# Optimization experiments

Measured on AMD Instinct MI355X. Metric: run time of the kernel, lower is better.

## Reference

```python
import jax, jax.numpy as jnp
import numpy as np
from jax import lax

B, L, C = 8, 2048, 512
H = 8
D = C // H  # head_dim = 64
FF = 4 * C


def layer_norm(x, g, b, eps=1e-5):
    mu = jnp.mean(x, axis=-1, keepdims=True)
    var = jnp.mean((x - mu) ** 2, axis=-1, keepdims=True)
    return (x - mu) * lax.rsqrt(var + eps) * g + b


def conv1d(x, w, b, groups=1):
    # x: [N, Cin, L], w: [Cout, Cin//groups, K], 'same' padding for K=3
    y = lax.conv_general_dilated(
        x, w, window_strides=(1,), padding=[(1, 1)],
        dimension_numbers=('NCH', 'OIH', 'NCH'), feature_group_count=groups)
    return y + b[None, :, None]


def setup_inputs() -> dict:
    key = jax.random.key(0)
    ks = jax.random.split(key, 12)
    s = 0.02
    inp = {
        'x': jax.random.normal(ks[0], (B, L, C), dtype=jnp.float32),
        # norm1
        'g1': jnp.ones((C,), jnp.float32), 'b1': jnp.zeros((C,), jnp.float32),
        # attention projections (stored as [in, out] for x @ W)
        'qk_w': jax.random.normal(ks[1], (C, 2 * C), jnp.float32) * s,
        'qk_b': jnp.zeros((2 * C,), jnp.float32),
        'v_w': jax.random.normal(ks[2], (C, C), jnp.float32) * s,
        'v_b': jnp.zeros((C,), jnp.float32),
        # depthwise LePE conv: [D, 1, 3], groups=D
        'lepe_w': jax.random.normal(ks[3], (D, 1, 3), jnp.float32) * s,
        'lepe_b': jnp.zeros((D,), jnp.float32),
        # norm2
        'g2': jnp.ones((C,), jnp.float32), 'b2': jnp.zeros((C,), jnp.float32),
        # GatedConv1D: inner LayerNorm + Conv1d(C, 2C, 3, pad=1); proj_out=Identity (expansion=1)
        'spn_g': jnp.ones((C,), jnp.float32), 'spn_b': jnp.zeros((C,), jnp.float32),
        'sp_cw': jax.random.normal(ks[4], (2 * C, C, 3), jnp.float32) * s,
        'sp_cb': jnp.zeros((2 * C,), jnp.float32),
        # norm3
        'g3': jnp.ones((C,), jnp.float32), 'b3': jnp.zeros((C,), jnp.float32),
        # FFN
        'w1': jax.random.normal(ks[5], (C, FF), jnp.float32) * s,
        'bb1': jnp.zeros((FF,), jnp.float32),
        'w2': jax.random.normal(ks[6], (FF, C), jnp.float32) * s,
        'bb2': jnp.zeros((C,), jnp.float32),
    }
    return inp


def _attn(x, qk_w, qk_b, v_w, v_b, lepe_w, lepe_b):
    # x: [B, L, C]
    qk = (x @ qk_w + qk_b).reshape(B, L, 2, H, D).transpose(2, 0, 3, 1, 4)
    q, k = qk[0], qk[1]                      # [B, H, L, D]
    v = (x @ v_w + v_b).reshape(B, L, H, D).transpose(0, 2, 1, 3)  # [B, H, L, D]
    q = jax.nn.elu(q) + 1.0
    k = jax.nn.elu(k) + 1.0

    def lepe(t):
        # Faithful to torch: raw row-major reshape [B,H,L,D] -> [B*H, D, L]
        # (NOT a transpose), depthwise conv along last axis, reshape back.
        c = conv1d(t.reshape(B * H, D, L), lepe_w, lepe_b, groups=D)
        return t + c.reshape(B, H, D, L).transpose(0, 1, 3, 2)

    q = lepe(q)
    k = lepe(k)
    k_mean = jnp.mean(k, axis=2, keepdims=True)                    # [B, H, 1, D]
    z = 1.0 / (jnp.einsum('bhld,bhmd->bhlm', q, k_mean) + 1e-6)    # [B, H, L, 1]
    kv = jnp.einsum('bhld,bhle->bhde', k, v) / L                   # [B, H, D, D]
    out = jnp.einsum('bhld,bhde->bhle', q, kv) * z                 # [B, H, L, D]
    return out.transpose(0, 2, 1, 3).reshape(B, L, C)


def reference(x, g1, b1, qk_w, qk_b, v_w, v_b, lepe_w, lepe_b,
              g2, b2, spn_g, spn_b, sp_cw, sp_cb, g3, b3, w1, bb1, w2, bb2):
    # Dropout is identity (eval mode).
    # Block 1: linear attention with LePE
    x = x + _attn(layer_norm(x, g1, b1), qk_w, qk_b, v_w, v_b, lepe_w, lepe_b)

    # Block 2: gated conv state path. state_path(input) = input + gated(conv(LN(input)))
    sp_in = layer_norm(x, g2, b2)
    h = layer_norm(sp_in, spn_g, spn_b)
    c = conv1d(h.transpose(0, 2, 1), sp_cw, sp_cb).transpose(0, 2, 1)  # [B, L, 2C]
    vv, gg = jnp.split(c, 2, axis=-1)
    x = x + (sp_in + vv * jax.nn.sigmoid(gg))

    # Block 3: FFN with exact GELU (torch default)
    h = layer_norm(x, g3, b3)
    x = x + (jax.nn.gelu(h @ w1 + bb1, approximate=False) @ w2 + bb2)
    return x
```

## Files before the change

### kernel.cpp

```cpp
#include <hip/hip_runtime.h>
#include <hip/hip_bf16.h>
#include <math.h>

#define Bb 8
#define Ll 2048
#define Ccn 512
#define Hh 8
#define Dd 64
#define NR (Bb * Ll)

typedef __hip_bfloat16 bf16;
typedef __attribute__((ext_vector_type(8))) __bf16 bf16x8;
typedef __attribute__((ext_vector_type(4))) float f32x4;

#define GLDS(g, l) __builtin_amdgcn_global_load_lds(                          \
    (const __attribute__((address_space(1))) void*)(g),                       \
    (__attribute__((address_space(3))) void*)(l), 16, 0, 0)

__device__ __forceinline__ void unpack2(unsigned u, float& a, float& b) {
  union { float f; unsigned x; } lo, hi;
  lo.x = u << 16; hi.x = u & 0xffff0000u;
  a = lo.f; b = hi.f;
}

__device__ __forceinline__ float ldin(const void* p, int i, int isbf) {
  return isbf ? (float)((const bf16*)p)[i] : ((const float*)p)[i];
}

__device__ __forceinline__ void ldin8(const void* p, size_t base, int isbf, float* v) {
  if (isbf) {
    int4 q = *(const int4*)((const bf16*)p + base);
    unpack2((unsigned)q.x, v[0], v[1]); unpack2((unsigned)q.y, v[2], v[3]);
    unpack2((unsigned)q.z, v[4], v[5]); unpack2((unsigned)q.w, v[6], v[7]);
  } else {
    float4 a = *(const float4*)((const float*)p + base);
    float4 b = *(const float4*)((const float*)p + base + 4);
    v[0]=a.x; v[1]=a.y; v[2]=a.z; v[3]=a.w;
    v[4]=b.x; v[5]=b.y; v[6]=b.z; v[7]=b.w;
  }
}

__device__ __forceinline__ void st8(bf16* dst, const float* v) {
  bf16x8 o;
#pragma unroll
  for (int t = 0; t < 8; ++t) o[t] = (__bf16)v[t];
  *(bf16x8*)dst = o;
}

__global__ void detect_kernel(const unsigned* __restrict__ g1, int* __restrict__ flag) {
  *flag = ((g1[0] & 0xFFFFu) == 0x3F80u) ? 1 : 0;
}

__global__ void ln1_kernel(const void* __restrict__ x, const void* __restrict__ g,
                           const void* __restrict__ b, const int* __restrict__ dflag,
                           bf16* __restrict__ outb, float* __restrict__ xf)
{
  int isbf = *dflag;
  int row  = blockIdx.x * 4 + (threadIdx.x >> 6);
  int lane = threadIdx.x & 63;
  size_t obase = (size_t)row * Ccn + lane * 8;
  float vals[8];
  ldin8(x, obase, isbf, vals);
  float4 c0 = {vals[0], vals[1], vals[2], vals[3]};
  float4 c1 = {vals[4], vals[5], vals[6], vals[7]};
  *(float4*)(xf + obase)     = c0;
  *(float4*)(xf + obase + 4) = c1;
  float s = 0.f, q = 0.f;
#pragma unroll
  for (int a = 0; a < 8; ++a) { s += vals[a]; q += vals[a] * vals[a]; }
#pragma unroll
  for (int off = 1; off < 64; off <<= 1) {
    s += __shfl_xor(s, off);
    q += __shfl_xor(q, off);
  }
  float mu  = s * (1.f / Ccn);
  float var = q * (1.f / Ccn) - mu * mu;
  float rs  = rsqrtf(var + 1e-5f);
  float gv[8], bv[8], o[8];
  ldin8(g, lane * 8, isbf, gv);
  ldin8(b, lane * 8, isbf, bv);
#pragma unroll
  for (int a = 0; a < 8; ++a) o[a] = (vals[a] - mu) * rs * gv[a] + bv[a];
  st8(&outb[obase], o);
}

__global__ void ln_kernel(const float* __restrict__ xin, const void* __restrict__ g,
                          const void* __restrict__ b, const int* __restrict__ dflag,
                          bf16* __restrict__ outb)
{
  int isbf = *dflag;
  int row  = blockIdx.x * 4 + (threadIdx.x >> 6);
  int lane = threadIdx.x & 63;
  const float* xr = xin + (size_t)row * Ccn;
  float4 v0 = *(const float4*)(xr + lane * 8);
  float4 v1 = *(const float4*)(xr + lane * 8 + 4);
  float vals[8] = {v0.x, v0.y, v0.z, v0.w, v1.x, v1.y, v1.z, v1.w};
  float s = 0.f, q = 0.f;
#pragma unroll
  for (int a = 0; a < 8; ++a) { s += vals[a]; q += vals[a] * vals[a]; }
#pragma unroll
  for (int off = 1; off < 64; off <<= 1) {
    s += __shfl_xor(s, off);
    q += __shfl_xor(q, off);
  }
  float mu  = s * (1.f / Ccn);
  float var = q * (1.f / Ccn) - mu * mu;
  float rs  = rsqrtf(var + 1e-5f);
  size_t obase = (size_t)row * Ccn + lane * 8;
  float gv[8], bv[8], o[8];
  ldin8(g, lane * 8, isbf, gv);
  ldin8(b, lane * 8, isbf, bv);
#pragma unroll
  for (int a = 0; a < 8; ++a) o[a] = (vals[a] - mu) * rs * gv[a] + bv[a];
  st8(&outb[obase], o);
}

__global__ void ln2_kernel(const float* __restrict__ xin, const void* __restrict__ g,
                           const void* __restrict__ b, const void* __restrict__ sg,
                           const void* __restrict__ sb, const int* __restrict__ dflag,
                           bf16* __restrict__ sp_out, bf16* __restrict__ h_out)
{
  int isbf = *dflag;
  int row  = blockIdx.x * 4 + (threadIdx.x >> 6);
  int lane = threadIdx.x & 63;
  const float* xr = xin + (size_t)row * Ccn;
  float4 v0 = *(const float4*)(xr + lane * 8);
  float4 v1 = *(const float4*)(xr + lane * 8 + 4);
  float vals[8] = {v0.x, v0.y, v0.z, v0.w, v1.x, v1.y, v1.z, v1.w};
  float s = 0.f, q = 0.f;
#pragma unroll
  for (int a = 0; a < 8; ++a) { s += vals[a]; q += vals[a] * vals[a]; }
#pragma unroll
  for (int off = 1; off < 64; off <<= 1) {
    s += __shfl_xor(s, off);
    q += __shfl_xor(q, off);
  }
  float mu  = s * (1.f / Ccn);
  float var = q * (1.f / Ccn) - mu * mu;
  float rs  = rsqrtf(var + 1e-5f);
  size_t obase = (size_t)row * Ccn + lane * 8;
  float gv[8], bv[8], o[8];
  ldin8(g, lane * 8, isbf, gv);
  ldin8(b, lane * 8, isbf, bv);
  float s2 = 0.f, q2 = 0.f;
#pragma unroll
  for (int a = 0; a < 8; ++a) {
    o[a] = (vals[a] - mu) * rs * gv[a] + bv[a];
    s2 += o[a]; q2 += o[a] * o[a];
  }
  st8(&sp_out[obase], o);
#pragma unroll
  for (int off = 1; off < 64; off <<= 1) {
    s2 += __shfl_xor(s2, off);
    q2 += __shfl_xor(q2, off);
  }
  float mu2  = s2 * (1.f / Ccn);
  float var2 = q2 * (1.f / Ccn) - mu2 * mu2;
  float rs2  = rsqrtf(var2 + 1e-5f);
  float sgv[8], sbv[8], o2[8];
  ldin8(sg, lane * 8, isbf, sgv);
  ldin8(sb, lane * 8, isbf, sbv);
#pragma unroll
  for (int a = 0; a < 8; ++a) o2[a] = (o[a] - mu2) * rs2 * sgv[a] + sbv[a];
  st8(&h_out[obase], o2);
}

__global__ void transpose_w(const void* __restrict__ src, bf16* __restrict__ dst,
                            const int* __restrict__ dflag, int R, int C) {
  int isbf = *dflag;
  __shared__ bf16 tile[32][33];
  int c0 = blockIdx.x * 32, r0 = blockIdx.y * 32;
  int tx = threadIdx.x & 31, ty = threadIdx.x >> 5;
#pragma unroll
  for (int i = 0; i < 32; i += 8)
    tile[ty + i][tx] = (bf16)ldin(src, (r0 + ty + i) * C + c0 + tx, isbf);
  __syncthreads();
#pragma unroll
  for (int i = 0; i < 32; i += 8)
    dst[(size_t)(c0 + ty + i) * R + r0 + tx] = tile[tx][ty + i];
}

__global__ void convw_permute(const void* __restrict__ src, bf16* __restrict__ dst,
                              const int* __restrict__ dflag) {
  int isbf = *dflag;
  int idx = blockIdx.x * 256 + threadIdx.x;
  int o = idx / 1536, j = idx - o * 1536;
  int k = j >> 9, i = j & 511;
  dst[idx] = (bf16)ldin(src, o * 1536 + i * 3 + k, isbf);
}

#define EPI_NONE  0
#define EPI_ELU1  1
#define EPI_GELU  2
#define EPI_RESID 3
#define EPI_QKV   4

template<int EPI, bool CONV>
__global__ void gemm_bt(const bf16* __restrict__ A, const bf16* __restrict__ Bt,
                        const void* __restrict__ bias, const void* __restrict__ bias2,
                        const float* __restrict__ resid,
                        void* __restrict__ out, void* __restrict__ out2,
                        const int* __restrict__ dflag,
                        int M, int Nn, int K, int orow0)
{
  int isbf = *dflag;
  __shared__ __align__(16) bf16 As[128 * 64];
  __shared__ __align__(16) bf16 Bs[128 * 64];
  int tid  = threadIdx.x;
  int wave = tid >> 6, lane = tid & 63;
  int wm = (wave >> 1) * 64, wn = (wave & 1) * 64;
  int row0 = blockIdx.x * 128;
  int col0 = blockIdx.y * 128;
  f32x4 acc[4][4] = {};
  int m_in = lane & 15;
  int kq   = lane >> 4;
  int r8   = lane >> 3;
  int swz8 = (((lane & 7) - r8) & 7) * 8;

  for (int k0 = 0; k0 < K; k0 += 64) {
    {
      int cw = col0 + wave * 32;
#pragma unroll
      for (int g = 0; g < 4; ++g)
        GLDS(&Bt[(size_t)(cw + g*8 + r8) * K + k0 + swz8], &Bs[(wave*32 + g*8) * 64]);
    }
    if (CONV) {
      int kpos = k0 >> 9;
      int ii   = (k0 & 511) + swz8;
#pragma unroll
      for (int g = 0; g < 4; ++g) {
        int rt = row0 + wave*32 + g*8 + r8;
        int rs = rt + kpos - 1;
        rs = rs < 0 ? 0 : (rs > M - 1 ? M - 1 : rs);
        GLDS(&A[(size_t)rs * 512 + ii], &As[(wave*32 + g*8) * 64]);
      }
    } else {
#pragma unroll
      for (int g = 0; g < 4; ++g)
        GLDS(&A[(size_t)(row0 + wave*32 + g*8 + r8) * K + k0 + swz8],
             &As[(wave*32 + g*8) * 64]);
    }
    __syncthreads();
    if (CONV) {
      int kpos = k0 >> 9;
      int bad = -1;
      if (kpos == 0 && (row0 & 2047) == 0)    bad = 0;
      if (kpos == 2 && (row0 & 2047) == 1920) bad = 127;
      if (bad >= 0) {
        if (tid < 8) { int4 z = {0,0,0,0}; *(int4*)&As[bad * 64 + tid * 8] = z; }
        __syncthreads();
      }
    }
#pragma unroll
    for (int kk = 0; kk < 2; ++kk) {
      int Cu = kk * 4 + kq;
      bf16x8 af[4], bfr[4];
#pragma unroll
      for (int i = 0; i < 4; ++i) {
        int R = wm + i * 16 + m_in;
        af[i] = *(const bf16x8*)&As[R * 64 + ((Cu + R) & 7) * 8];
      }
#pragma unroll
      for (int j = 0; j < 4; ++j) {
        int R = wn + j * 16 + m_in;
        bfr[j] = *(const bf16x8*)&Bs[R * 64 + ((Cu + R) & 7) * 8];
      }
#pragma unroll
      for (int i = 0; i < 4; ++i)
#pragma unroll
        for (int j = 0; j < 4; ++j)
          acc[i][j] = __builtin_amdgcn_mfma_f32_16x16x32_bf16(af[i], bfr[j], acc[i][j], 0, 0, 0);
    }
    __syncthreads();
  }

  const int ESTR = 72;
  bf16* eb = As + wave * (16 * ESTR);
  int col_in = lane & 15;
  int row_in = (lane >> 4) * 4;
  int rr = lane >> 3;
  int cb = (lane & 7) * 8;
#pragma unroll
  for (int i = 0; i < 4; ++i) {
#pragma unroll
    for (int j = 0; j < 4; ++j) {
      int col = col0 + wn + j * 16 + col_in;
      float bv = (EPI == EPI_QKV)
          ? ((col < 1024) ? ldin(bias, col, isbf) : ldin(bias2, col - 1024, isbf))
          : ldin(bias, col, isbf);
#pragma unroll
      for (int r = 0; r < 4; ++r) {
        float v = acc[i][j][r] + bv;
        if (EPI == EPI_ELU1) v = (v > 0.f) ? (v + 1.f) : __expf(v);
        if (EPI == EPI_QKV && col < 1024) v = (v > 0.f) ? (v + 1.f) : __expf(v);
        if (EPI == EPI_GELU) {
          float u = v * (0.7978845608f + 0.0356774081f * v * v);
          u = fminf(fmaxf(u, -10.f), 10.f);
          float e = __expf(2.f * u);
          v = v * e / (e + 1.f);
        }
        eb[(row_in + r) * ESTR + j * 16 + col_in] = (bf16)v;
      }
    }
    int row = row0 + wm + i * 16;
#pragma unroll
    for (int s = 0; s < 2; ++s) {
      int r2 = rr + s * 8;
      bf16x8 pk = *(const bf16x8*)&eb[r2 * ESTR + cb];
      int grow = row + r2;
      int col  = col0 + wn + cb;
      if (EPI == EPI_RESID) {
        size_t gbase = (size_t)(grow + orow0) * Nn + col;
        float4 ra = *(const float4*)&resid[gbase];
        float4 rb = *(const float4*)&resid[gbase + 4];
        float vv[8];
#pragma unroll
        for (int t = 0; t < 8; ++t) vv[t] = (float)pk[t];
        vv[0]+=ra.x; vv[1]+=ra.y; vv[2]+=ra.z; vv[3]+=ra.w;
        vv[4]+=rb.x; vv[5]+=rb.y; vv[6]+=rb.z; vv[7]+=rb.w;
        if (isbf) {
          st8(&((bf16*)out)[gbase], vv);
        } else {
          float4 o0 = {vv[0], vv[1], vv[2], vv[3]};
          float4 o1 = {vv[4], vv[5], vv[6], vv[7]};
          *(float4*)&((float*)out)[gbase]     = o0;
          *(float4*)&((float*)out)[gbase + 4] = o1;
        }
      } else if (EPI == EPI_QKV) {
        if (col < 1024)
          *(bf16x8*)&((bf16*)out)[(size_t)grow * 1024 + col] = pk;
        else
          *(bf16x8*)&((bf16*)out2)[(size_t)grow * 512 + (col - 1024)] = pk;
      } else {
        *(bf16x8*)&((bf16*)out)[(size_t)grow * Nn + col] = pk;
      }
    }
  }
}

template<int SRCOFF, int DSTSTR>
__global__ void lepe2_kernel(const bf16* __restrict__ qk, bf16* __restrict__ dst,
                             const void* __restrict__ w, const void* __restrict__ cb,
                             const int* __restrict__ dflag) {
  int isbf = *dflag;
  __shared__ float buf[64][66];
  int bh = blockIdx.y; int b = bh >> 3, h = bh & 7;
  int tile = blockIdx.x;
  int t = threadIdx.x;
  int r  = t >> 3;
  int o8 = (t & 7) * 8;
  size_t sbase = (size_t)b * 2048 * 1024 + SRCOFF + h * 64;

  int4 cv[2], id[2];
#pragma unroll
  for (int it = 0; it < 2; ++it) {
    int ch = r + it * 32;
    cv[it] = *(const int4*)&qk[sbase + (size_t)(ch * 32 + tile) * 1024 + o8];
    id[it] = *(const int4*)&qk[sbase + (size_t)(tile * 64 + ch) * 1024 + o8];
  }
  float edge = 0.f; int eidx = -1, espot = 0;
  if (t < 64) {
    eidx = t; espot = 0;
    if (tile > 0) edge = (float)qk[sbase + (size_t)(t * 32 + tile - 1) * 1024 + 63];
  } else if (t < 128) {
    eidx = t - 64; espot = 65;
    if (tile < 31) edge = (float)qk[sbase + (size_t)((t - 64) * 32 + tile + 1) * 1024 + 0];
  }
  float w0[2], w1[2], w2[2], bi[2];
#pragma unroll
  for (int it = 0; it < 2; ++it) {
    int ch = r + it * 32;
    w0[it] = ldin(w, ch * 3 + 0, isbf);
    w1[it] = ldin(w, ch * 3 + 1, isbf);
    w2[it] = ldin(w, ch * 3 + 2, isbf);
    bi[it] = ldin(cb, ch, isbf);
  }
#pragma unroll
  for (int it = 0; it < 2; ++it) {
    float v[8];
    unpack2((unsigned)cv[it].x, v[0], v[1]); unpack2((unsigned)cv[it].y, v[2], v[3]);
    unpack2((unsigned)cv[it].z, v[4], v[5]); unpack2((unsigned)cv[it].w, v[6], v[7]);
    int ch = r + it * 32;
#pragma unroll
    for (int k = 0; k < 8; ++k) buf[ch][1 + o8 + k] = v[k];
  }
  if (eidx >= 0) buf[eidx][espot] = edge;
  __syncthreads();
  float co[2][8];
#pragma unroll
  for (int it = 0; it < 2; ++it) {
    int ch = r + it * 32;
    float a0 = buf[ch][o8], a1 = buf[ch][o8 + 1];
#pragma unroll
    for (int k = 0; k < 8; ++k) {
      float a2 = buf[ch][o8 + 2 + k];
      co[it][k] = bi[it] + w0[it] * a0 + w1[it] * a1 + w2[it] * a2;
      a0 = a1; a1 = a2;
    }
  }
  __syncthreads();
#pragma unroll
  for (int it = 0; it < 2; ++it) {
    int ch = r + it * 32;
#pragma unroll
    for (int k = 0; k < 8; ++k) buf[o8 + k][ch] = co[it][k];
  }
  __syncthreads();
#pragma unroll
  for (int it = 0; it < 2; ++it) {
    int lr = r + it * 32;
    float v[8];
    unpack2((unsigned)id[it].x, v[0], v[1]); unpack2((unsigned)id[it].y, v[2], v[3]);
    unpack2((unsigned)id[it].z, v[4], v[5]); unpack2((unsigned)id[it].w, v[6], v[7]);
#pragma unroll
    for (int k = 0; k < 8; ++k) v[k] += buf[lr][o8 + k];
    st8(&dst[(size_t)(b * 2048 + tile * 64 + lr) * DSTSTR + h * 64 + o8], v);
  }
}

__global__ void kmean_kernel(const bf16* __restrict__ k2, float* __restrict__ kmean) {
  int bh = blockIdx.x, ls = blockIdx.y;
  int b = bh >> 3, h = bh & 7;
  int t = threadIdx.x; int d = t & 63, part = t >> 6;
  float s = 0.f;
  int l0 = ls * 256 + part * 64;
#pragma unroll 4
  for (int i = 0; i < 64; ++i)
    s += (float)k2[((size_t)(b*2048 + l0 + i)) * 1024 + h*64 + d];
  __shared__ float red[256];
  red[t] = s; __syncthreads();
  if (t < 64)
    atomicAdd(&kmean[bh*64 + d], (red[d] + red[64+d] + red[128+d] + red[192+d]) * (1.f/2048.f));
}

__global__ void kv_kernel(const bf16* __restrict__ k2, const bf16* __restrict__ v,
                          float* __restrict__ kv) {
  int bh = blockIdx.x, split = blockIdx.y;
  int b = bh >> 3, h = bh & 7;
  int t = threadIdx.x;
  __shared__ __align__(16) bf16 ks[64][64];
  __shared__ __align__(16) bf16 vs[64][64];
  int d0 = (t & 15) * 4, e0 = (t >> 4) * 4;
  int lr = t >> 2, q4 = (t & 3) * 16;
  float acc[4][4] = {};
  for (int chunk = 0; chunk < 4; ++chunk) {
    int l = split * 256 + chunk * 64 + lr;
    size_t rk = ((size_t)(b*2048 + l)) * 1024 + h*64 + q4;
    size_t rv = ((size_t)(b*2048 + l)) * 512 + h*64 + q4;
    *(int4*)&ks[lr][q4]     = *(const int4*)&k2[rk];
    *(int4*)&ks[lr][q4 + 8] = *(const int4*)&k2[rk + 8];
    *(int4*)&vs[lr][q4]     = *(const int4*)&v[rv];
    *(int4*)&vs[lr][q4 + 8] = *(const int4*)&v[rv + 8];
    __syncthreads();
    for (int l2 = 0; l2 < 64; ++l2) {
      float kvv[4], vvv[4];
#pragma unroll
      for (int a = 0; a < 4; ++a) kvv[a] = (float)ks[l2][d0 + a];
#pragma unroll
      for (int a = 0; a < 4; ++a) vvv[a] = (float)vs[l2][e0 + a];
#pragma unroll
      for (int a = 0; a < 4; ++a)
#pragma unroll
        for (int c = 0; c < 4; ++c) acc[a][c] += kvv[a] * vvv[c];
    }
    __syncthreads();
  }
  const float sc = 1.f / 2048.f;
#pragma unroll
  for (int a = 0; a < 4; ++a)
#pragma unroll
    for (int c = 0; c < 4; ++c)
      atomicAdd(&kv[(size_t)(bh*64 + d0 + a) * 64 + e0 + c], acc[a][c] * sc);
}

__global__ void attn_out_kernel(const bf16* __restrict__ q2, const float* __restrict__ kv,
                                const float* __restrict__ kmean, float* __restrict__ xf) {
  int bh = blockIdx.x; int b = bh >> 3, h = bh & 7;
  int lbase = blockIdx.y * 64;
  int t = threadIdx.x;
  __shared__ float kvs[64][65];
  __shared__ float km[64];
  for (int i = t; i < 64*64; i += 256) kvs[i >> 6][i & 63] = kv[(size_t)bh*4096 + i];
  if (t < 64) km[t] = kmean[bh*64 + t];
  __syncthreads();
  int lr = t >> 2, eg = (t & 3) * 16;
  int l = lbase + lr;
  size_t qrow = ((size_t)(b*2048 + l)) * 512 + h*64;
  float qv[64];
#pragma unroll
  for (int d8 = 0; d8 < 64; d8 += 8) {
    int4 p = *(const int4*)&q2[qrow + d8];
    unpack2((unsigned)p.x, qv[d8+0], qv[d8+1]);
    unpack2((unsigned)p.y, qv[d8+2], qv[d8+3]);
    unpack2((unsigned)p.z, qv[d8+4], qv[d8+5]);
    unpack2((unsigned)p.w, qv[d8+6], qv[d8+7]);
  }
  float zd = 0.f;
#pragma unroll
  for (int d = 0; d < 64; ++d) zd += qv[d] * km[d];
  float z = 1.f / (zd + 1e-6f);
  float sacc[16] = {};
#pragma unroll
  for (int d = 0; d < 64; ++d) {
    float qd = qv[d];
    const float* row = &kvs[d][eg];
#pragma unroll
    for (int i = 0; i < 16; ++i) sacc[i] += qd * row[i];
  }
  size_t xrow = ((size_t)(b*2048 + l)) * 512 + h*64 + eg;
#pragma unroll
  for (int s = 0; s < 4; ++s) {
    float4 cur = *(const float4*)&xf[xrow + s * 4];
    cur.x += sacc[s*4+0] * z; cur.y += sacc[s*4+1] * z;
    cur.z += sacc[s*4+2] * z; cur.w += sacc[s*4+3] * z;
    *(float4*)&xf[xrow + s * 4] = cur;
  }
}

__global__ void gating_kernel(float* __restrict__ xf, const bf16* __restrict__ spin,
                              const bf16* __restrict__ c) {
  size_t idx = ((size_t)blockIdx.x * 256 + threadIdx.x) * 8;
  size_t n = idx >> 9; int cc = (int)(idx & 511);
  float vv[8], gg[8], sp[8];
  ldin8(&c[n * 1024 + cc], 0, 1, vv);
  ldin8(&c[n * 1024 + 512 + cc], 0, 1, gg);
  ldin8(&spin[idx], 0, 1, sp);
#pragma unroll
  for (int s = 0; s < 2; ++s) {
    float4 cur = *(const float4*)&xf[idx + s * 4];
    float* cp = &cur.x;
#pragma unroll
    for (int t = 0; t < 4; ++t) {
      int a = s * 4 + t;
      cp[t] += sp[a] + vv[a] / (1.f + __expf(-gg[a]));
    }
    *(float4*)&xf[idx + s * 4] = cur;
  }
}

extern "C" void kernel_launch(void* const* d_in, const int* in_sizes, int n_in,
                              void* d_out, int out_size, void* d_ws, size_t ws_size,
                              hipStream_t stream) {
  (void)in_sizes; (void)n_in; (void)out_size;
  const void* x      = d_in[0];
  const void* g1     = d_in[1];
  const void* b1     = d_in[2];
  const void* qk_w   = d_in[3];
  const void* qk_b   = d_in[4];
  const void* v_w    = d_in[5];
  const void* v_b    = d_in[6];
  const void* lepe_w = d_in[7];
  const void* lepe_b = d_in[8];
  const void* g2     = d_in[9];
  const void* b2     = d_in[10];
  const void* spn_g  = d_in[11];
  const void* spn_b  = d_in[12];
  const void* sp_cw  = d_in[13];
  const void* sp_cb  = d_in[14];
  const void* g3     = d_in[15];
  const void* b3     = d_in[16];
  const void* w1     = d_in[17];
  const void* bb1    = d_in[18];
  const void* w2     = d_in[19];
  const void* bb2    = d_in[20];

  char* ws = (char*)d_ws;
  const size_t MB = 1 << 20;
  const bool big = ws_size >= (size_t)129 * MB;

  bf16*  qk_wT  = (bf16*)(ws);
  bf16*  v_wT   = (bf16*)(ws + 0x100000);
  bf16*  convWT = (bf16*)(ws + 0x180000);
  bf16*  w1T    = (bf16*)(ws + 0x480000);
  bf16*  w2T    = (bf16*)(ws + 0x680000);
  float* kmean  = (float*)(ws + 0x880000);
  float* kvb    = (float*)(ws + 0x890000);
  int*   dflag  = (int*)(ws + 0x990000);
  float* xf     = (float*)(ws + 16*MB);
  bf16*  ybf    = (bf16*)(ws + 48*MB);
  bf16*  qkbuf  = (bf16*)(ws + 64*MB);
  bf16*  spbuf  = ybf;
  bf16*  ybf2   = (bf16*)(ws + 64*MB);
  bf16*  cbufS  = (bf16*)(ws + 80*MB);
  bf16*  cbufB  = (bf16*)(ws + 96*MB);
  bf16*  tbuf   = (bf16*)(ws + 64*MB);
  bf16*  vout   = (bf16*)d_out;

  detect_kernel<<<1, 1, 0, stream>>>((const unsigned*)g1, dflag);
  hipMemsetAsync(kvb, 0, 64 * 64 * 64 * sizeof(float), stream);
  hipMemsetAsync(kmean, 0, 64 * 64 * sizeof(float), stream);

  transpose_w<<<dim3(32, 16), 256, 0, stream>>>(qk_w, qk_wT, dflag, 512, 1024);
  transpose_w<<<dim3(16, 16), 256, 0, stream>>>(v_w,  v_wT,  dflag, 512, 512);
  transpose_w<<<dim3(64, 16), 256, 0, stream>>>(w1,   w1T,   dflag, 512, 2048);
  transpose_w<<<dim3(16, 64), 256, 0, stream>>>(w2,   w2T,   dflag, 2048, 512);
  convw_permute<<<1024*1536/256, 256, 0, stream>>>(sp_cw, convWT, dflag);

  ln1_kernel<<<NR/4, 256, 0, stream>>>(x, g1, b1, dflag, ybf, xf);
  gemm_bt<EPI_QKV, false><<<dim3(128, 12), 256, 0, stream>>>(
      ybf, qk_wT, qk_b, v_b, nullptr, qkbuf, vout, dflag, NR, 1536, 512, 0);
  lepe2_kernel<0,   512 ><<<dim3(32, 64), 256, 0, stream>>>(qkbuf, ybf,   lepe_w, lepe_b, dflag);
  lepe2_kernel<512, 1024><<<dim3(32, 64), 256, 0, stream>>>(qkbuf, qkbuf, lepe_w, lepe_b, dflag);
  kmean_kernel<<<dim3(64, 8), 256, 0, stream>>>(qkbuf, kmean);
  kv_kernel<<<dim3(64, 8), 256, 0, stream>>>(qkbuf, vout, kvb);
  attn_out_kernel<<<dim3(64, 32), 256, 0, stream>>>(ybf, kvb, kmean, xf);

  ln2_kernel<<<NR/4, 256, 0, stream>>>(xf, g2, b2, spn_g, spn_b, dflag, spbuf, ybf2);
  if (big) {
    gemm_bt<EPI_NONE, true><<<dim3(128, 8), 256, 0, stream>>>(
        ybf2, convWT, sp_cb, nullptr, nullptr, cbufB, nullptr, dflag, NR, 1024, 1536, 0);
    gating_kernel<<<NR*512/2048, 256, 0, stream>>>(xf, spbuf, cbufB);
  } else {
    for (int half = 0; half < 2; ++half) {
      size_t ro = (size_t)half * 8192;
      gemm_bt<EPI_NONE, true><<<dim3(64, 8), 256, 0, stream>>>(
          ybf2 + ro*512, convWT, sp_cb, nullptr, nullptr, cbufS, nullptr, dflag, 8192, 1024, 1536, 0);
      gating_kernel<<<8192*512/2048, 256, 0, stream>>>(xf + ro*512, spbuf + ro*512, cbufS);
    }
  }

  ln_kernel<<<NR/4, 256, 0, stream>>>(xf, g3, b3, dflag, ybf);
  if (big) {
    gemm_bt<EPI_GELU,  false><<<dim3(128, 16), 256, 0, stream>>>(
        ybf, w1T, bb1, nullptr, nullptr, tbuf, nullptr, dflag, NR, 2048, 512, 0);
    gemm_bt<EPI_RESID, false><<<dim3(128, 4),  256, 0, stream>>>(
        tbuf, w2T, bb2, nullptr, xf, d_out, nullptr, dflag, NR, 512, 2048, 0);
  } else {
    for (int half = 0; half < 2; ++half) {
      size_t ro = (size_t)half * 8192;
      gemm_bt<EPI_GELU,  false><<<dim3(64, 16), 256, 0, stream>>>(
          ybf + ro*512, w1T, bb1, nullptr, nullptr, tbuf, nullptr, dflag, 8192, 2048, 512, 0);
      gemm_bt<EPI_RESID, false><<<dim3(64, 4),  256, 0, stream>>>(
          tbuf, w2T, bb2, nullptr, xf, d_out, nullptr, dflag, 8192, 512, 2048, (int)ro);
    }
  }
}
```

Before: 538.6 us.

## Triple-buffer GEMM mainloop with async LDS loads and padded conv input

Replaces the single-buffered GEMM mainloop (load, barrier, compute, barrier per 64-wide K step) with a three-stage ring of 32-wide K tiles. Global-to-LDS loads are issued two steps ahead and throttled with vmcnt waits, so memory latency overlaps MFMA work and one barrier per step is removed. It also remaps workgroups with an XCD-aware swizzle, sets launch bounds for three blocks per CU, and raises MFMA priority. The conv input is now written into a per-batch buffer padded with zeroed guard rows, which removes the clamping and the boundary-zeroing barrier in the conv GEMM at the cost of a small extra kernel and a workspace layout change.

```diff
diff --git a/kernel.cpp b/kernel.cpp
--- a/kernel.cpp
+++ b/kernel.cpp
@@ -8,6 +8,7 @@
 #define Hh 8
 #define Dd 64
 #define NR (Bb * Ll)
+#define PROW 2050
 
 typedef __hip_bfloat16 bf16;
 typedef __attribute__((ext_vector_type(8))) __bf16 bf16x8;
@@ -162,7 +163,17 @@
   ldin8(sb, lane * 8, isbf, sbv);
 #pragma unroll
   for (int a = 0; a < 8; ++a) o2[a] = (o[a] - mu2) * rs2 * sgv[a] + sbv[a];
-  st8(&h_out[obase], o2);
+  size_t prow = (size_t)(row >> 11) * PROW + 1 + (row & 2047);
+  st8(&h_out[prow * Ccn + lane * 8], o2);
+}
+
+__global__ void guard_zero(bf16* __restrict__ P) {
+  int b = blockIdx.x;
+  int t = threadIdx.x;
+  size_t r0 = (size_t)b * PROW * Ccn;
+  size_t r1 = r0 + (size_t)(PROW - 1) * Ccn;
+  ((int*)(P + r0))[t] = 0;
+  ((int*)(P + r1))[t] = 0;
 }
 
 __global__ void transpose_w(const void* __restrict__ src, bf16* __restrict__ dst,
@@ -196,86 +207,93 @@
 #define EPI_QKV   4
 
 template<int EPI, bool CONV>
-__global__ void gemm_bt(const bf16* __restrict__ A, const bf16* __restrict__ Bt,
-                        const void* __restrict__ bias, const void* __restrict__ bias2,
-                        const float* __restrict__ resid,
-                        void* __restrict__ out, void* __restrict__ out2,
-                        const int* __restrict__ dflag,
-                        int M, int Nn, int K, int orow0)
+__global__ __launch_bounds__(256, 3)
+void gemm_pl(const bf16* __restrict__ A, const bf16* __restrict__ Bt,
+             const void* __restrict__ bias, const void* __restrict__ bias2,
+             const float* __restrict__ resid,
+             void* __restrict__ out, void* __restrict__ out2,
+             const int* __restrict__ dflag,
+             int M, int Nn, int K, int orow0)
 {
   int isbf = *dflag;
-  __shared__ __align__(16) bf16 As[128 * 64];
-  __shared__ __align__(16) bf16 Bs[128 * 64];
+  __shared__ __align__(16) bf16 lds[3 * 8192];
   int tid  = threadIdx.x;
   int wave = tid >> 6, lane = tid & 63;
+
+  int gdx = gridDim.x;
+  int nwg = gdx * (int)gridDim.y;
+  int lin = (int)blockIdx.y * gdx + (int)blockIdx.x;
+  lin = (lin & 7) * (nwg >> 3) + (lin >> 3);
+  int row0 = (lin % gdx) * 128;
+  int col0 = (lin / gdx) * 128;
+
   int wm = (wave >> 1) * 64, wn = (wave & 1) * 64;
-  int row0 = blockIdx.x * 128;
-  int col0 = blockIdx.y * 128;
   f32x4 acc[4][4] = {};
   int m_in = lane & 15;
   int kq   = lane >> 4;
-  int r8   = lane >> 3;
-  int swz8 = (((lane & 7) - r8) & 7) * 8;
-
-  for (int k0 = 0; k0 < K; k0 += 64) {
-    {
-      int cw = col0 + wave * 32;
-#pragma unroll
-      for (int g = 0; g < 4; ++g)
-        GLDS(&Bt[(size_t)(cw + g*8 + r8) * K + k0 + swz8], &Bs[(wave*32 + g*8) * 64]);
-    }
-    if (CONV) {
-      int kpos = k0 >> 9;
-      int ii   = (k0 & 511) + swz8;
-#pragma unroll
-      for (int g = 0; g < 4; ++g) {
-        int rt = row0 + wave*32 + g*8 + r8;
-        int rs = rt + kpos - 1;
-        rs = rs < 0 ? 0 : (rs > M - 1 ? M - 1 : rs);
-        GLDS(&A[(size_t)rs * 512 + ii], &As[(wave*32 + g*8) * 64]);
-      }
-    } else {
-#pragma unroll
-      for (int g = 0; g < 4; ++g)
-        GLDS(&A[(size_t)(row0 + wave*32 + g*8 + r8) * K + k0 + swz8],
-             &As[(wave*32 + g*8) * 64]);
-    }
-    __syncthreads();
-    if (CONV) {
-      int kpos = k0 >> 9;
-      int bad = -1;
-      if (kpos == 0 && (row0 & 2047) == 0)    bad = 0;
-      if (kpos == 2 && (row0 & 2047) == 1920) bad = 127;
-      if (bad >= 0) {
-        if (tid < 8) { int4 z = {0,0,0,0}; *(int4*)&As[bad * 64 + tid * 8] = z; }
-        __syncthreads();
-      }
-    }
-#pragma unroll
-    for (int kk = 0; kk < 2; ++kk) {
-      int Cu = kk * 4 + kq;
-      bf16x8 af[4], bfr[4];
-#pragma unroll
-      for (int i = 0; i < 4; ++i) {
-        int R = wm + i * 16 + m_in;
-        af[i] = *(const bf16x8*)&As[R * 64 + ((Cu + R) & 7) * 8];
-      }
-#pragma unroll
-      for (int j = 0; j < 4; ++j) {
-        int R = wn + j * 16 + m_in;
-        bfr[j] = *(const bf16x8*)&Bs[R * 64 + ((Cu + R) & 7) * 8];
-      }
-#pragma unroll
-      for (int i = 0; i < 4; ++i)
-#pragma unroll
-        for (int j = 0; j < 4; ++j)
-          acc[i][j] = __builtin_amdgcn_mfma_f32_16x16x32_bf16(af[i], bfr[j], acc[i][j], 0, 0, 0);
-    }
-    __syncthreads();
-  }
+
+  int srow = lane >> 2;
+  int scol = (((lane & 3) - (srow & 3)) & 3) * 8;
+  size_t ars;
+  size_t arow;
+  if (CONV) {
+    ars = 512;
+    int bb = row0 >> 11, l0 = row0 & 2047;
+    arow = (size_t)bb * PROW + l0 + wave * 32 + srow;
+  } else {
+    ars = (size_t)K;
+    arow = (size_t)row0 + wave * 32 + srow;
+  }
+  const bf16* Ap = A  + arow * ars + scol;
+  const bf16* Bp = Bt + ((size_t)col0 + wave * 32 + srow) * K + scol;
+  bf16* ldsA = &lds[(wave * 32) * 32];
+  bf16* ldsB = &lds[4096 + (wave * 32) * 32];
+  int NT = K >> 5;
+
+#define STAGE_PL(koff, bofs) do {                                             \
+    GLDS(Ap + (koff),                  ldsA + (bofs));                        \
+    GLDS(Ap + (koff) + 16 * ars,       ldsA + (bofs) + 16 * 32);              \
+    GLDS(Bp + (koff),                  ldsB + (bofs));                        \
+    GLDS(Bp + (koff) + 16 * (size_t)K, ldsB + (bofs) + 16 * 32);              \
+  } while (0)
+
+  STAGE_PL(0, 0);
+  STAGE_PL(32, 8192);
+  int bco = 0, bso = 16384;
+  for (int t = 0; t < NT; ++t) {
+    if (t + 1 < NT) { asm volatile("s_waitcnt vmcnt(4)" ::: "memory"); }
+    else            { asm volatile("s_waitcnt vmcnt(0)" ::: "memory"); }
+    __builtin_amdgcn_sched_barrier(0);
+    asm volatile("" ::: "memory");
+    __builtin_amdgcn_s_barrier();
+    asm volatile("" ::: "memory");
+    __builtin_amdgcn_sched_barrier(0);
+    if (t + 2 < NT) STAGE_PL((size_t)(t + 2) * 32, bso);
+    bf16x8 af[4], bfr[4];
+#pragma unroll
+    for (int i = 0; i < 4; ++i) {
+      int R = wm + i * 16 + m_in;
+      af[i] = *(const bf16x8*)&lds[bco + R * 32 + ((kq + R) & 3) * 8];
+    }
+#pragma unroll
+    for (int j = 0; j < 4; ++j) {
+      int R = wn + j * 16 + m_in;
+      bfr[j] = *(const bf16x8*)&lds[bco + 4096 + R * 32 + ((kq + R) & 3) * 8];
+    }
+    __builtin_amdgcn_s_setprio(1);
+#pragma unroll
+    for (int i = 0; i < 4; ++i)
+#pragma unroll
+      for (int j = 0; j < 4; ++j)
+        acc[i][j] = __builtin_amdgcn_mfma_f32_16x16x32_bf16(af[i], bfr[j], acc[i][j], 0, 0, 0);
+    __builtin_amdgcn_s_setprio(0);
+    bco = (bco == 16384) ? 0 : bco + 8192;
+    bso = (bso == 16384) ? 0 : bso + 8192;
+  }
+  __syncthreads();
 
   const int ESTR = 72;
-  bf16* eb = As + wave * (16 * ESTR);
+  bf16* eb = lds + wave * (16 * ESTR);
   int col_in = lane & 15;
   int row_in = (lane >> 4) * 4;
   int rr = lane >> 3;
@@ -336,6 +354,7 @@
       }
     }
   }
+#undef STAGE_PL
 }
 
 template<int SRCOFF, int DSTSTR>
@@ -580,8 +599,8 @@
   bf16*  ybf    = (bf16*)(ws + 48*MB);
   bf16*  qkbuf  = (bf16*)(ws + 64*MB);
   bf16*  spbuf  = ybf;
-  bf16*  ybf2   = (bf16*)(ws + 64*MB);
-  bf16*  cbufS  = (bf16*)(ws + 80*MB);
+  bf16*  ybf2p  = (bf16*)(ws + 64*MB);
+  bf16*  cbufS  = (bf16*)(ws + 96*MB);
   bf16*  cbufB  = (bf16*)(ws + 96*MB);
   bf16*  tbuf   = (bf16*)(ws + 64*MB);
   bf16*  vout   = (bf16*)d_out;
@@ -597,7 +616,7 @@
   convw_permute<<<1024*1536/256, 256, 0, stream>>>(sp_cw, convWT, dflag);
 
   ln1_kernel<<<NR/4, 256, 0, stream>>>(x, g1, b1, dflag, ybf, xf);
-  gemm_bt<EPI_QKV, false><<<dim3(128, 12), 256, 0, stream>>>(
+  gemm_pl<EPI_QKV, false><<<dim3(128, 12), 256, 0, stream>>>(
       ybf, qk_wT, qk_b, v_b, nullptr, qkbuf, vout, dflag, NR, 1536, 512, 0);
   lepe2_kernel<0,   512 ><<<dim3(32, 64), 256, 0, stream>>>(qkbuf, ybf,   lepe_w, lepe_b, dflag);
   lepe2_kernel<512, 1024><<<dim3(32, 64), 256, 0, stream>>>(qkbuf, qkbuf, lepe_w, lepe_b, dflag);
@@ -605,32 +624,34 @@
   kv_kernel<<<dim3(64, 8), 256, 0, stream>>>(qkbuf, vout, kvb);
   attn_out_kernel<<<dim3(64, 32), 256, 0, stream>>>(ybf, kvb, kmean, xf);
 
-  ln2_kernel<<<NR/4, 256, 0, stream>>>(xf, g2, b2, spn_g, spn_b, dflag, spbuf, ybf2);
+  guard_zero<<<8, 256, 0, stream>>>(ybf2p);
+  ln2_kernel<<<NR/4, 256, 0, stream>>>(xf, g2, b2, spn_g, spn_b, dflag, spbuf, ybf2p);
   if (big) {
-    gemm_bt<EPI_NONE, true><<<dim3(128, 8), 256, 0, stream>>>(
-        ybf2, convWT, sp_cb, nullptr, nullptr, cbufB, nullptr, dflag, NR, 1024, 1536, 0);
+    gemm_pl<EPI_NONE, true><<<dim3(128, 8), 256, 0, stream>>>(
+        ybf2p, convWT, sp_cb, nullptr, nullptr, cbufB, nullptr, dflag, NR, 1024, 1536, 0);
     gating_kernel<<<NR*512/2048, 256, 0, stream>>>(xf, spbuf, cbufB);
   } else {
     for (int half = 0; half < 2; ++half) {
       size_t ro = (size_t)half * 8192;
-      gemm_bt<EPI_NONE, true><<<dim3(64, 8), 256, 0, stream>>>(
-          ybf2 + ro*512, convWT, sp_cb, nullptr, nullptr, cbufS, nullptr, dflag, 8192, 1024, 1536, 0);
+      gemm_pl<EPI_NONE, true><<<dim3(64, 8), 256, 0, stream>>>(
+          ybf2p + (ro >> 11) * PROW * 512, convWT, sp_cb, nullptr, nullptr,
+          cbufS, nullptr, dflag, 8192, 1024, 1536, 0);
       gating_kernel<<<8192*512/2048, 256, 0, stream>>>(xf + ro*512, spbuf + ro*512, cbufS);
     }
   }
 
   ln_kernel<<<NR/4, 256, 0, stream>>>(xf, g3, b3, dflag, ybf);
   if (big) {
-    gemm_bt<EPI_GELU,  false><<<dim3(128, 16), 256, 0, stream>>>(
+    gemm_pl<EPI_GELU,  false><<<dim3(128, 16), 256, 0, stream>>>(
         ybf, w1T, bb1, nullptr, nullptr, tbuf, nullptr, dflag, NR, 2048, 512, 0);
-    gemm_bt<EPI_RESID, false><<<dim3(128, 4),  256, 0, stream>>>(
+    gemm_pl<EPI_RESID, false><<<dim3(128, 4),  256, 0, stream>>>(
         tbuf, w2T, bb2, nullptr, xf, d_out, nullptr, dflag, NR, 512, 2048, 0);
   } else {
     for (int half = 0; half < 2; ++half) {
       size_t ro = (size_t)half * 8192;
-      gemm_bt<EPI_GELU,  false><<<dim3(64, 16), 256, 0, stream>>>(
+      gemm_pl<EPI_GELU,  false><<<dim3(64, 16), 256, 0, stream>>>(
           ybf + ro*512, w1T, bb1, nullptr, nullptr, tbuf, nullptr, dflag, 8192, 2048, 512, 0);
-      gemm_bt<EPI_RESID, false><<<dim3(64, 4),  256, 0, stream>>>(
+      gemm_pl<EPI_RESID, false><<<dim3(64, 4),  256, 0, stream>>>(
           tbuf, w2T, bb2, nullptr, xf, d_out, nullptr, dflag, 8192, 512, 2048, (int)ro);
     }
   }
```

After: 565.4 us. +5.0%, slower.

## Pad conv input rows, fuse gating with LN3, and fold k-mean into LePE

Applied to the files above, without the earlier changes.

The conv GEMM's input is now written into a per-batch padded buffer with zeroed guard rows. This removes the clamped row indexing and the extra LDS zeroing plus barrier at sequence edges. The gating step and the third LayerNorm are fused into one kernel in the large-workspace path, saving a full read/write pass over the fp32 residual. The k-mean reduction moves into the K LePE kernel through partial sums and atomics, which removes a separate pass over K but adds two barriers to that kernel. The padded buffer needs a small guard-zeroing launch and changes the workspace layout.

```diff
diff --git a/kernel.cpp b/kernel.cpp
--- a/kernel.cpp
+++ b/kernel.cpp
@@ -8,6 +8,7 @@
 #define Hh 8
 #define Dd 64
 #define NR (Bb * Ll)
+#define PROW 2050
 
 typedef __hip_bfloat16 bf16;
 typedef __attribute__((ext_vector_type(8))) __bf16 bf16x8;
@@ -115,6 +116,49 @@
   st8(&outb[obase], o);
 }
 
+__global__ void glng_kernel(float* __restrict__ xf, const bf16* __restrict__ spin,
+                            const bf16* __restrict__ c, const void* __restrict__ g,
+                            const void* __restrict__ b, const int* __restrict__ dflag,
+                            bf16* __restrict__ outb)
+{
+  int isbf = *dflag;
+  int row  = blockIdx.x * 4 + (threadIdx.x >> 6);
+  int lane = threadIdx.x & 63;
+  size_t obase = (size_t)row * Ccn + lane * 8;
+  int cc = lane * 8;
+  float vv[8], gg[8], sp[8], xv[8];
+  ldin8(&c[(size_t)row * 1024 + cc], 0, 1, vv);
+  ldin8(&c[(size_t)row * 1024 + 512 + cc], 0, 1, gg);
+  ldin8(&spin[obase], 0, 1, sp);
+  float4 a0 = *(const float4*)&xf[obase];
+  float4 a1 = *(const float4*)&xf[obase + 4];
+  xv[0]=a0.x; xv[1]=a0.y; xv[2]=a0.z; xv[3]=a0.w;
+  xv[4]=a1.x; xv[5]=a1.y; xv[6]=a1.z; xv[7]=a1.w;
+#pragma unroll
+  for (int a = 0; a < 8; ++a) xv[a] += sp[a] + vv[a] / (1.f + __expf(-gg[a]));
+  float4 o0 = {xv[0], xv[1], xv[2], xv[3]};
+  float4 o1 = {xv[4], xv[5], xv[6], xv[7]};
+  *(float4*)&xf[obase]     = o0;
+  *(float4*)&xf[obase + 4] = o1;
+  float s = 0.f, q = 0.f;
+#pragma unroll
+  for (int a = 0; a < 8; ++a) { s += xv[a]; q += xv[a] * xv[a]; }
+#pragma unroll
+  for (int off = 1; off < 64; off <<= 1) {
+    s += __shfl_xor(s, off);
+    q += __shfl_xor(q, off);
+  }
+  float mu  = s * (1.f / Ccn);
+  float var = q * (1.f / Ccn) - mu * mu;
+  float rs  = rsqrtf(var + 1e-5f);
+  float gv[8], bv[8], o[8];
+  ldin8(g, lane * 8, isbf, gv);
+  ldin8(b, lane * 8, isbf, bv);
+#pragma unroll
+  for (int a = 0; a < 8; ++a) o[a] = (xv[a] - mu) * rs * gv[a] + bv[a];
+  st8(&outb[obase], o);
+}
+
 __global__ void ln2_kernel(const float* __restrict__ xin, const void* __restrict__ g,
                            const void* __restrict__ b, const void* __restrict__ sg,
                            const void* __restrict__ sb, const int* __restrict__ dflag,
@@ -162,7 +206,17 @@
   ldin8(sb, lane * 8, isbf, sbv);
 #pragma unroll
   for (int a = 0; a < 8; ++a) o2[a] = (o[a] - mu2) * rs2 * sgv[a] + sbv[a];
-  st8(&h_out[obase], o2);
+  size_t prow = (size_t)(row >> 11) * PROW + 1 + (row & 2047);
+  st8(&h_out[prow * Ccn + lane * 8], o2);
+}
+
+__global__ void guard_zero(bf16* __restrict__ P) {
+  int b = blockIdx.x;
+  int t = threadIdx.x;
+  size_t r0 = (size_t)b * PROW * Ccn;
+  size_t r1 = r0 + (size_t)(PROW - 1) * Ccn;
+  ((int*)(P + r0))[t] = 0;
+  ((int*)(P + r1))[t] = 0;
 }
 
 __global__ void transpose_w(const void* __restrict__ src, bf16* __restrict__ dst,
@@ -216,6 +270,11 @@
   int kq   = lane >> 4;
   int r8   = lane >> 3;
   int swz8 = (((lane & 7) - r8) & 7) * 8;
+  size_t prow0 = 0;
+  if (CONV) {
+    int bb = row0 >> 11, l0 = row0 & 2047;
+    prow0 = (size_t)bb * PROW + l0;
+  }
 
   for (int k0 = 0; k0 < K; k0 += 64) {
     {
@@ -229,10 +288,8 @@
       int ii   = (k0 & 511) + swz8;
 #pragma unroll
       for (int g = 0; g < 4; ++g) {
-        int rt = row0 + wave*32 + g*8 + r8;
-        int rs = rt + kpos - 1;
-        rs = rs < 0 ? 0 : (rs > M - 1 ? M - 1 : rs);
-        GLDS(&A[(size_t)rs * 512 + ii], &As[(wave*32 + g*8) * 64]);
+        size_t rs = prow0 + wave*32 + g*8 + r8 + kpos;
+        GLDS(&A[rs * 512 + ii], &As[(wave*32 + g*8) * 64]);
       }
     } else {
 #pragma unroll
@@ -241,16 +298,6 @@
              &As[(wave*32 + g*8) * 64]);
     }
     __syncthreads();
-    if (CONV) {
-      int kpos = k0 >> 9;
-      int bad = -1;
-      if (kpos == 0 && (row0 & 2047) == 0)    bad = 0;
-      if (kpos == 2 && (row0 & 2047) == 1920) bad = 127;
-      if (bad >= 0) {
-        if (tid < 8) { int4 z = {0,0,0,0}; *(int4*)&As[bad * 64 + tid * 8] = z; }
-        __syncthreads();
-      }
-    }
 #pragma unroll
     for (int kk = 0; kk < 2; ++kk) {
       int Cu = kk * 4 + kq;
@@ -338,10 +385,10 @@
   }
 }
 
-template<int SRCOFF, int DSTSTR>
+template<int SRCOFF, int DSTSTR, bool DOKM>
 __global__ void lepe2_kernel(const bf16* __restrict__ qk, bf16* __restrict__ dst,
                              const void* __restrict__ w, const void* __restrict__ cb,
-                             const int* __restrict__ dflag) {
+                             const int* __restrict__ dflag, float* __restrict__ km) {
   int isbf = *dflag;
   __shared__ float buf[64][66];
   int bh = blockIdx.y; int b = bh >> 3, h = bh & 7;
@@ -406,6 +453,9 @@
     for (int k = 0; k < 8; ++k) buf[o8 + k][ch] = co[it][k];
   }
   __syncthreads();
+  float psum[8];
+#pragma unroll
+  for (int k = 0; k < 8; ++k) psum[k] = 0.f;
 #pragma unroll
   for (int it = 0; it < 2; ++it) {
     int lr = r + it * 32;
@@ -413,24 +463,24 @@
     unpack2((unsigned)id[it].x, v[0], v[1]); unpack2((unsigned)id[it].y, v[2], v[3]);
     unpack2((unsigned)id[it].z, v[4], v[5]); unpack2((unsigned)id[it].w, v[6], v[7]);
 #pragma unroll
-    for (int k = 0; k < 8; ++k) v[k] += buf[lr][o8 + k];
+    for (int k = 0; k < 8; ++k) {
+      v[k] += buf[lr][o8 + k];
+      if (DOKM) psum[k] += v[k];
+    }
     st8(&dst[(size_t)(b * 2048 + tile * 64 + lr) * DSTSTR + h * 64 + o8], v);
   }
-}
-
-__global__ void kmean_kernel(const bf16* __restrict__ k2, float* __restrict__ kmean) {
-  int bh = blockIdx.x, ls = blockIdx.y;
-  int b = bh >> 3, h = bh & 7;
-  int t = threadIdx.x; int d = t & 63, part = t >> 6;
-  float s = 0.f;
-  int l0 = ls * 256 + part * 64;
-#pragma unroll 4
-  for (int i = 0; i < 64; ++i)
-    s += (float)k2[((size_t)(b*2048 + l0 + i)) * 1024 + h*64 + d];
-  __shared__ float red[256];
-  red[t] = s; __syncthreads();
-  if (t < 64)
-    atomicAdd(&kmean[bh*64 + d], (red[d] + red[64+d] + red[128+d] + red[192+d]) * (1.f/2048.f));
+  if (DOKM) {
+    __syncthreads();
+#pragma unroll
+    for (int k = 0; k < 8; ++k) buf[r][o8 + k] = psum[k];
+    __syncthreads();
+    if (t < 64) {
+      float s = 0.f;
+#pragma unroll 8
+      for (int rr2 = 0; rr2 < 32; ++rr2) s += buf[rr2][t];
+      atomicAdd(&km[bh * 64 + t], s * (1.f / 2048.f));
+    }
+  }
 }
 
 __global__ void kv_kernel(const bf16* __restrict__ k2, const bf16* __restrict__ v,
@@ -580,8 +630,8 @@
   bf16*  ybf    = (bf16*)(ws + 48*MB);
   bf16*  qkbuf  = (bf16*)(ws + 64*MB);
   bf16*  spbuf  = ybf;
-  bf16*  ybf2   = (bf16*)(ws + 64*MB);
-  bf16*  cbufS  = (bf16*)(ws + 80*MB);
+  bf16*  ybf2p  = (bf16*)(ws + 64*MB);
+  bf16*  cbufS  = (bf16*)(ws + 96*MB);
   bf16*  cbufB  = (bf16*)(ws + 96*MB);
   bf16*  tbuf   = (bf16*)(ws + 64*MB);
   bf16*  vout   = (bf16*)d_out;
@@ -599,27 +649,30 @@
   ln1_kernel<<<NR/4, 256, 0, stream>>>(x, g1, b1, dflag, ybf, xf);
   gemm_bt<EPI_QKV, false><<<dim3(128, 12), 256, 0, stream>>>(
       ybf, qk_wT, qk_b, v_b, nullptr, qkbuf, vout, dflag, NR, 1536, 512, 0);
-  lepe2_kernel<0,   512 ><<<dim3(32, 64), 256, 0, stream>>>(qkbuf, ybf,   lepe_w, lepe_b, dflag);
-  lepe2_kernel<512, 1024><<<dim3(32, 64), 256, 0, stream>>>(qkbuf, qkbuf, lepe_w, lepe_b, dflag);
-  kmean_kernel<<<dim3(64, 8), 256, 0, stream>>>(qkbuf, kmean);
+  lepe2_kernel<0,   512,  false><<<dim3(32, 64), 256, 0, stream>>>(
+      qkbuf, ybf, lepe_w, lepe_b, dflag, nullptr);
+  lepe2_kernel<512, 1024, true ><<<dim3(32, 64), 256, 0, stream>>>(
+      qkbuf, qkbuf, lepe_w, lepe_b, dflag, kmean);
   kv_kernel<<<dim3(64, 8), 256, 0, stream>>>(qkbuf, vout, kvb);
   attn_out_kernel<<<dim3(64, 32), 256, 0, stream>>>(ybf, kvb, kmean, xf);
 
-  ln2_kernel<<<NR/4, 256, 0, stream>>>(xf, g2, b2, spn_g, spn_b, dflag, spbuf, ybf2);
+  guard_zero<<<8, 256, 0, stream>>>(ybf2p);
+  ln2_kernel<<<NR/4, 256, 0, stream>>>(xf, g2, b2, spn_g, spn_b, dflag, spbuf, ybf2p);
   if (big) {
     gemm_bt<EPI_NONE, true><<<dim3(128, 8), 256, 0, stream>>>(
-        ybf2, convWT, sp_cb, nullptr, nullptr, cbufB, nullptr, dflag, NR, 1024, 1536, 0);
-    gating_kernel<<<NR*512/2048, 256, 0, stream>>>(xf, spbuf, cbufB);
+        ybf2p, convWT, sp_cb, nullptr, nullptr, cbufB, nullptr, dflag, NR, 1024, 1536, 0);
+    glng_kernel<<<NR/4, 256, 0, stream>>>(xf, spbuf, cbufB, g3, b3, dflag, ybf);
   } else {
     for (int half = 0; half < 2; ++half) {
       size_t ro = (size_t)half * 8192;
       gemm_bt<EPI_NONE, true><<<dim3(64, 8), 256, 0, stream>>>(
-          ybf2 + ro*512, convWT, sp_cb, nullptr, nullptr, cbufS, nullptr, dflag, 8192, 1024, 1536, 0);
+          ybf2p + (ro >> 11) * PROW * 512, convWT, sp_cb, nullptr, nullptr,
+          cbufS, nullptr, dflag, 8192, 1024, 1536, 0);
       gating_kernel<<<8192*512/2048, 256, 0, stream>>>(xf + ro*512, spbuf + ro*512, cbufS);
     }
-  }
-
-  ln_kernel<<<NR/4, 256, 0, stream>>>(xf, g3, b3, dflag, ybf);
+    ln_kernel<<<NR/4, 256, 0, stream>>>(xf, g3, b3, dflag, ybf);
+  }
+
   if (big) {
     gemm_bt<EPI_GELU,  false><<<dim3(128, 16), 256, 0, stream>>>(
         ybf, w1T, bb1, nullptr, nullptr, tbuf, nullptr, dflag, NR, 2048, 512, 0);
```

New measurement: 523.7 us. 1.03x faster.
